# Kernel tuning notes

Measured on AMD Instinct MI355X. Metric: run time of the kernel, lower is better.

## Reference

```python
import jax, jax.numpy as jnp
import numpy as np

C = 64
B, H, W = 2, 128, 512
SCALE = C ** (-0.5)


def conv1x1(x, w, b):
    # x: [B,C,H,W], w: [O,I], b: [O]
    return jnp.einsum('bihw,oi->bohw', x, w) + b[None, :, None, None]


def dwconv3x3(x, w, b):
    # depthwise 3x3, w: [C,1,3,3]
    y = jax.lax.conv_general_dilated(
        x, w, window_strides=(1, 1), padding='SAME',
        feature_group_count=x.shape[1],
        dimension_numbers=('NCHW', 'OIHW', 'NCHW'))
    return y + b[None, :, None, None]


def proj12(x, w1, b1, wd, bd):
    return dwconv3x3(conv1x1(x, w1, b1), wd, bd)


def setup_inputs() -> dict:
    key = jax.random.key(0)
    ks = jax.random.split(key, 32)
    d = {}
    d['x_l'] = jax.random.normal(ks[0], (B, C, H, W), dtype=jnp.float32)
    d['x_r'] = jax.random.normal(ks[1], (B, C, H, W), dtype=jnp.float32)
    i = 2
    for p in ['lp1', 'rp1', 'lp2', 'rp2']:
        d[p + '_w1'] = jax.random.normal(ks[i], (C, C), dtype=jnp.float32) * 0.05; i += 1
        d[p + '_b1'] = jnp.zeros((C,), dtype=jnp.float32)
        d[p + '_wd'] = jax.random.normal(ks[i], (C, 1, 3, 3), dtype=jnp.float32) * 0.1; i += 1
        d[p + '_bd'] = jnp.zeros((C,), dtype=jnp.float32)
    for p in ['lp3', 'rp3']:
        d[p + '_w'] = jax.random.normal(ks[i], (C, C), dtype=jnp.float32) * 0.05; i += 1
        d[p + '_b'] = jnp.zeros((C,), dtype=jnp.float32)
    return d


def reference(x_l, x_r,
              lp1_w1, lp1_b1, lp1_wd, lp1_bd,
              rp1_w1, rp1_b1, rp1_wd, rp1_bd,
              lp2_w1, lp2_b1, lp2_wd, lp2_bd,
              rp2_w1, rp2_b1, rp2_wd, rp2_bd,
              lp3_w, lp3_b, rp3_w, rp3_b):
    Ql = proj12(x_l, lp1_w1, lp1_b1, lp1_wd, lp1_bd)  # [B,C,H,W]
    Qr = proj12(x_r, rp1_w1, rp1_b1, rp1_wd, rp1_bd)  # [B,C,H,W]
    # attention[b,h,w,v] = sum_c Ql[b,c,h,w] * Qr[b,c,h,v]
    att = jnp.einsum('bchw,bchv->bhwv', Ql, Qr) * SCALE  # [B,H,W,W]
    Vl = proj12(x_l, lp2_w1, lp2_b1, lp2_wd, lp2_bd)
    Vr = proj12(x_r, rp2_w1, rp2_b1, rp2_wd, rp2_bd)
    # softmax over right-view width (last axis), aggregate Vr
    A_r2l = jax.nn.softmax(att, axis=-1)
    F_r2l = jnp.einsum('bhwv,bchv->bchw', A_r2l, Vr)  # [B,C,H,W]
    # transposed attention, softmax over left-view width (axis -2 of att)
    A_l2r = jax.nn.softmax(att, axis=-2)
    F_l2r = jnp.einsum('bhwv,bchw->bchv', A_l2r, Vl)  # [B,C,H,W]
    F_r2l = conv1x1(F_r2l, lp3_w, lp3_b)
    F_l2r = conv1x1(F_l2r, rp3_w, rp3_b)
    return x_l + F_r2l + x_r + F_l2r
```

## Files before the change

### kernel.cpp

```cpp
#include <hip/hip_runtime.h>
#include <hip/hip_bf16.h>

typedef __attribute__((ext_vector_type(8))) short short8;
typedef __attribute__((ext_vector_type(4))) float f32x4;

#define QSCALE 0.18033688011112042f

__device__ __forceinline__ unsigned short f2bf(float f){
    unsigned u = __float_as_uint(f);
    unsigned r = (u + 0x7fffu + ((u>>16)&1u))>>16;
    return (unsigned short)r;
}
__device__ __forceinline__ unsigned pk_rtne(float hi, float lo){
    return (((unsigned)f2bf(hi))<<16) | (unsigned)f2bf(lo);
}

__global__ __launch_bounds__(256) void prepgemm_k(const float* __restrict__ xl,
                                                  const float* __restrict__ xr,
                                                  float* __restrict__ out,
                                                  const float* __restrict__ wAL, const float* __restrict__ bAL,
                                                  const float* __restrict__ wBL, const float* __restrict__ bBL,
                                                  const float* __restrict__ wAR, const float* __restrict__ bAR,
                                                  const float* __restrict__ wBR, const float* __restrict__ bBR,
                                                  unsigned short* __restrict__ T1L, unsigned short* __restrict__ T2L,
                                                  unsigned short* __restrict__ T1R, unsigned short* __restrict__ T2R){
    __shared__ float ftA[64*130];
    __shared__ __align__(16) short sB[128*72];
    __shared__ float sbias[128];

    int bid = blockIdx.x;
    int b = bid >> 9, px0 = (bid & 511) << 7;
    int tid = threadIdx.x;
    int wv = tid>>6, lane = tid&63, quad = lane>>4, l16 = lane&15;

    float4 vxr[8];
    #pragma unroll
    for (int it=0; it<8; it++){
        int lin = it*256 + tid;
        int c = lin >> 5, piece = lin & 31;
        size_t off = (((size_t)(b*64 + c))<<16) + px0 + piece*4;
        float4 va = *(const float4*)(xl + off);
        float4 vb = *(const float4*)(xr + off);
        vxr[it] = vb;
        float4 vo; vo.x=va.x+vb.x; vo.y=va.y+vb.y; vo.z=va.z+vb.z; vo.w=va.w+vb.w;
        *(float4*)(out + off) = vo;
        float* d = ftA + c*130 + piece*4;
        float2 lo; lo.x=va.x; lo.y=va.y;
        float2 hi; hi.x=va.z; hi.y=va.w;
        *(float2*)(d) = lo;
        *(float2*)(d+2) = hi;
    }
    {
        #pragma unroll
        for (int it=0; it<8; it++){
            int lin = it*256 + tid;
            int o = lin >> 4, cc4 = (lin & 15) << 2;
            const float* wsrc = (o < 64) ? (wAL + o*64 + cc4) : (wBL + (o-64)*64 + cc4);
            float4 w4 = *(const float4*)wsrc;
            uint2 v; v.x = pk_rtne(w4.y, w4.x); v.y = pk_rtne(w4.w, w4.z);
            *(uint2*)(sB + o*72 + cc4) = v;
        }
        if (tid < 128) sbias[tid] = (tid < 64) ? bAL[tid] : bBL[tid-64];
    }
    __syncthreads();

    const f32x4 z4 = {0.f,0.f,0.f,0.f};

    #define DO_GEMM(T1p, T2p) do {                                                  \
        short8 a0[2], a1[2];                                                        \
        _Pragma("unroll")                                                           \
        for (int mt=0; mt<2; mt++){                                                 \
            int pxr = wv*32 + mt*16 + l16;                                          \
            _Pragma("unroll")                                                       \
            for (int j=0;j<8;j++){                                                  \
                a0[mt][j] = (short)f2bf(ftA[(quad*8 + j)*130 + pxr]);               \
                a1[mt][j] = (short)f2bf(ftA[(32 + quad*8 + j)*130 + pxr]);          \
            }                                                                       \
        }                                                                           \
        _Pragma("unroll")                                                           \
        for (int set=0; set<2; set++){                                              \
            unsigned short* T = set ? (T2p) : (T1p);                                \
            short8 bB0[4], bB1[4];                                                  \
            _Pragma("unroll")                                                       \
            for (int nt=0; nt<4; nt++){                                             \
                bB0[nt] = *(const short8*)(sB + (set*64 + nt*16 + l16)*72 + quad*8);      \
                bB1[nt] = *(const short8*)(sB + (set*64 + nt*16 + l16)*72 + 32 + quad*8); \
            }                                                                       \
            _Pragma("unroll")                                                       \
            for (int nt=0; nt<4; nt++){                                             \
                float4 b4 = *(const float4*)(sbias + set*64 + nt*16 + quad*4);      \
                _Pragma("unroll")                                                   \
                for (int mt=0; mt<2; mt++){                                         \
                    f32x4 acc = __builtin_amdgcn_mfma_f32_16x16x32_bf16(bB0[nt], a0[mt], z4, 0,0,0); \
                    acc       = __builtin_amdgcn_mfma_f32_16x16x32_bf16(bB1[nt], a1[mt], acc, 0,0,0); \
                    uint2 v;                                                        \
                    v.x = pk_rtne(acc[1]+b4.y, acc[0]+b4.x);                        \
                    v.y = pk_rtne(acc[3]+b4.w, acc[2]+b4.z);                        \
                    int px = px0 + wv*32 + mt*16 + l16;                             \
                    *(uint2*)(T + (size_t)px*64 + nt*16 + quad*4) = v;              \
                }                                                                   \
            }                                                                       \
        }                                                                           \
    } while(0)

    DO_GEMM(T1L + ((size_t)b<<22), T2L + ((size_t)b<<22));
    __syncthreads();

    #pragma unroll
    for (int it=0; it<8; it++){
        int lin = it*256 + tid;
        int c = lin >> 5, piece = lin & 31;
        float4 vb = vxr[it];
        float* d = ftA + c*130 + piece*4;
        float2 lo; lo.x=vb.x; lo.y=vb.y;
        float2 hi; hi.x=vb.z; hi.y=vb.w;
        *(float2*)(d) = lo;
        *(float2*)(d+2) = hi;
    }
    {
        #pragma unroll
        for (int it=0; it<8; it++){
            int lin = it*256 + tid;
            int o = lin >> 4, cc4 = (lin & 15) << 2;
            const float* wsrc = (o < 64) ? (wAR + o*64 + cc4) : (wBR + (o-64)*64 + cc4);
            float4 w4 = *(const float4*)wsrc;
            uint2 v; v.x = pk_rtne(w4.y, w4.x); v.y = pk_rtne(w4.w, w4.z);
            *(uint2*)(sB + o*72 + cc4) = v;
        }
        if (tid < 128) sbias[tid] = (tid < 64) ? bAR[tid] : bBR[tid-64];
    }
    __syncthreads();

    DO_GEMM(T1R + ((size_t)b<<22), T2R + ((size_t)b<<22));
    #undef DO_GEMM
}

__device__ __forceinline__ void dw_tile(const unsigned short* __restrict__ Tb,
                                        const float* __restrict__ wd,
                                        const float* __restrict__ bd,
                                        int c0, int w0, int h, float acc[4][4]){
    #pragma unroll
    for (int ch=0; ch<4; ch++){
        float bv = bd[c0+ch];
        #pragma unroll
        for (int i=0;i<4;i++) acc[ch][i] = bv;
    }
    #pragma unroll
    for (int dh=-1; dh<=1; dh++){
        int hh = h + dh;
        if (hh < 0 || hh > 127) continue;
        const unsigned short* Tr = Tb + ((size_t)(hh*512))*64 + c0;
        float win[6][4];
        #pragma unroll
        for (int j=0;j<6;j++){
            int ww = w0 - 1 + j;
            if (ww >= 0 && ww < 512){
                uint2 v = *(const uint2*)(Tr + (size_t)ww*64);
                win[j][0] = __uint_as_float(v.x<<16);
                win[j][1] = __uint_as_float(v.x & 0xffff0000u);
                win[j][2] = __uint_as_float(v.y<<16);
                win[j][3] = __uint_as_float(v.y & 0xffff0000u);
            } else {
                win[j][0]=0.f; win[j][1]=0.f; win[j][2]=0.f; win[j][3]=0.f;
            }
        }
        #pragma unroll
        for (int ch=0; ch<4; ch++){
            float k0 = wd[(c0+ch)*9 + (dh+1)*3];
            float k1 = wd[(c0+ch)*9 + (dh+1)*3 + 1];
            float k2 = wd[(c0+ch)*9 + (dh+1)*3 + 2];
            #pragma unroll
            for (int i=0;i<4;i++)
                acc[ch][i] += k0*win[i][ch] + k1*win[i+1][ch] + k2*win[i+2][ch];
        }
    }
}

__global__ __launch_bounds__(256) void dwconv_k(const unsigned short* __restrict__ T1,
                                                const unsigned short* __restrict__ T2,
                                                const float* __restrict__ wd1,
                                                const float* __restrict__ bd1,
                                                const float* __restrict__ wd2,
                                                const float* __restrict__ bd2,
                                                unsigned short* __restrict__ Qdst,
                                                unsigned short* __restrict__ Vdst,
                                                float qscale){
    int bid = blockIdx.x;
    int wt = bid & 7, h = (bid>>3)&127, b = bid>>10;
    int tid = threadIdx.x;
    int cg = tid & 15, wl = tid >> 4;
    int c0 = cg*4;
    int w0 = wt*64 + wl*4;
    float acc[4][4];
    dw_tile(T1 + ((size_t)b<<22), wd1, bd1, c0, w0, h, acc);
    {
        int base = (b*128 + h)*512;
        #pragma unroll
        for (int i=0;i<4;i++){
            uint2 v;
            v.x = pk_rtne(acc[1][i]*qscale, acc[0][i]*qscale);
            v.y = pk_rtne(acc[3][i]*qscale, acc[2][i]*qscale);
            *(uint2*)(Qdst + ((size_t)(base + w0 + i))*64 + c0) = v;
        }
    }
    dw_tile(T2 + ((size_t)b<<22), wd2, bd2, c0, w0, h, acc);
    {
        #pragma unroll
        for (int ch=0; ch<4; ch++){
            uint2 v;
            v.x = pk_rtne(acc[ch][1], acc[ch][0]);
            v.y = pk_rtne(acc[ch][3], acc[ch][2]);
            *(uint2*)(Vdst + (((size_t)(b*64 + c0 + ch))<<16) + h*512 + w0) = v;
        }
    }
}

#define PQ 72
#define PK 72
#define PV 72
#define PP 72
#define PFA 72
#define POT 17
#define OFF_Q   0
#define OFF_K   18432
#define OFF_V   27648
#define LDS_TOT 36864

__global__ __launch_bounds__(256) void flash_k(
    const unsigned short* __restrict__ Ql, const unsigned short* __restrict__ Qr,
    const unsigned short* __restrict__ Vl, const unsigned short* __restrict__ Vr,
    const float* __restrict__ lw3, const float* __restrict__ lb3,
    const float* __restrict__ rw3, const float* __restrict__ rb3,
    float* __restrict__ out)
{
    __shared__ __align__(16) char smem[LDS_TOT];
    short* sK  = (short*)(smem + OFF_K);
    short* sV  = (short*)(smem + OFF_V);
    short* sP  = (short*)(smem + OFF_Q);
    short* sFA = (short*)(smem + OFF_Q);
    float* sOT = (float*)(smem + OFF_K);

    int bid = blockIdx.x;
    int g  = ((bid >> 5) << 3) | (bid & 7);
    int qt = (bid >> 3) & 3;
    int h = g & 127, b = (g >> 7) & 1, dir = g >> 8;
    const unsigned short *Qg, *Kg, *Vg; const float *w3, *b3;
    if (dir==0){ Qg = Ql; Kg = Qr; Vg = Vr; w3 = lw3; b3 = lb3; }
    else       { Qg = Qr; Kg = Ql; Vg = Vl; w3 = rw3; b3 = rb3; }

    int tid = threadIdx.x;
    int wv = tid>>6, lane = tid&63, quad = lane>>4, l16 = lane&15;
    int bh = b*128 + h;

    short8 aq0[2], aq1[2];
    #pragma unroll
    for (int s=0; s<2; s++){
        size_t qrow = ((size_t)bh*512 + qt*128 + wv*32 + s*16 + l16)*64;
        aq0[s] = *(const short8*)(Qg + qrow + quad*8);
        aq1[s] = *(const short8*)(Qg + qrow + 32 + quad*8);
    }

    const f32x4 z4 = {0.f,0.f,0.f,0.f};
    f32x4 oacc[2][4];
    #pragma unroll
    for (int s=0; s<2; s++)
        #pragma unroll
        for (int ct=0; ct<4; ct++) oacc[s][ct] = z4;
    float lps[2] = {0.f, 0.f};

    const uint4* Ksrc = (const uint4*)(Kg + (size_t)bh*512*64);
    const unsigned short* Vbase = Vg + ((size_t)(b*64)*128 + h)*512;

    for (int kt=0; kt<8; kt++){
        #pragma unroll
        for (int it=0; it<2; it++){
            int idx = it*256 + tid;
            int row = idx>>3, piece = idx&7;
            *(uint4*)(sK + row*PK + piece*8) = Ksrc[(size_t)(kt*64 + row)*8 + piece];
            uint4 vv = *(const uint4*)(Vbase + (size_t)row*65536 + kt*64 + piece*8);
            *(uint4*)(sV + row*PV + piece*8) = vv;
        }
        __syncthreads();
        #pragma unroll
        for (int nt=0; nt<4; nt++){
            short8 bk0 = *(const short8*)(sK + (nt*16 + l16)*PK + quad*8);
            short8 bk1 = *(const short8*)(sK + (nt*16 + l16)*PK + 32 + quad*8);
            #pragma unroll
            for (int s=0; s<2; s++){
                __builtin_amdgcn_s_setprio(1);
                f32x4 sv = __builtin_amdgcn_mfma_f32_16x16x32_bf16(bk0, aq0[s], z4, 0,0,0);
                sv       = __builtin_amdgcn_mfma_f32_16x16x32_bf16(bk1, aq1[s], sv, 0,0,0);
                __builtin_amdgcn_s_setprio(0);
                float p0 = __builtin_amdgcn_exp2f(sv[0]);
                float p1 = __builtin_amdgcn_exp2f(sv[1]);
                float p2 = __builtin_amdgcn_exp2f(sv[2]);
                float p3 = __builtin_amdgcn_exp2f(sv[3]);
                lps[s] += (p0+p1) + (p2+p3);
                unsigned lo = __builtin_amdgcn_perm(__float_as_uint(p1), __float_as_uint(p0), 0x07060302);
                unsigned hi = __builtin_amdgcn_perm(__float_as_uint(p3), __float_as_uint(p2), 0x07060302);
                uint2 pv; pv.x = lo; pv.y = hi;
                *(uint2*)(sP + (wv*32 + s*16 + l16)*PP + nt*16 + quad*4) = pv;
            }
        }
        short8 ap0[2], ap1[2];
        #pragma unroll
        for (int s=0; s<2; s++){
            ap0[s] = *(const short8*)(sP + (wv*32 + s*16 + l16)*PP + quad*8);
            ap1[s] = *(const short8*)(sP + (wv*32 + s*16 + l16)*PP + 32 + quad*8);
        }
        __builtin_amdgcn_s_setprio(1);
        #pragma unroll
        for (int ct=0; ct<4; ct++){
            short8 bv0 = *(const short8*)(sV + (ct*16 + l16)*PV + quad*8);
            short8 bv1 = *(const short8*)(sV + (ct*16 + l16)*PV + 32 + quad*8);
            #pragma unroll
            for (int s=0; s<2; s++){
                oacc[s][ct] = __builtin_amdgcn_mfma_f32_16x16x32_bf16(ap0[s], bv0, oacc[s][ct], 0,0,0);
                oacc[s][ct] = __builtin_amdgcn_mfma_f32_16x16x32_bf16(ap1[s], bv1, oacc[s][ct], 0,0,0);
            }
        }
        __builtin_amdgcn_s_setprio(0);
        __syncthreads();
    }

    float inv[2][4];
    #pragma unroll
    for (int s=0; s<2; s++){
        float l = lps[s];
        l += __shfl_xor(l, 16);
        l += __shfl_xor(l, 32);
        #pragma unroll
        for (int r=0;r<4;r++) inv[s][r] = 1.0f / __shfl(l, quad*4 + r);
    }

    #pragma unroll
    for (int s=0; s<2; s++){
        short* sFw = sFA + (wv*32 + s*16)*PFA;
        #pragma unroll
        for (int ct=0; ct<4; ct++){
            #pragma unroll
            for (int r=0;r<4;r++)
                sFw[(quad*4+r)*PFA + ct*16 + l16] = (short)f2bf(oacc[s][ct][r]*inv[s][r]);
        }
    }
    short8 af0[2], af1[2];
    #pragma unroll
    for (int s=0; s<2; s++){
        af0[s] = *(const short8*)(sFA + (wv*32 + s*16 + l16)*PFA + quad*8);
        af1[s] = *(const short8*)(sFA + (wv*32 + s*16 + l16)*PFA + 32 + quad*8);
    }
    f32x4 d2[2][4];
    #pragma unroll
    for (int ot=0; ot<4; ot++){
        const float* wrow = w3 + (ot*16 + l16)*64 + quad*8;
        float4 wa = *(const float4*)(wrow);
        float4 wb = *(const float4*)(wrow + 4);
        float4 wc = *(const float4*)(wrow + 32);
        float4 wd = *(const float4*)(wrow + 36);
        short8 bw0, bw1;
        bw0[0]=(short)f2bf(wa.x); bw0[1]=(short)f2bf(wa.y); bw0[2]=(short)f2bf(wa.z); bw0[3]=(short)f2bf(wa.w);
        bw0[4]=(short)f2bf(wb.x); bw0[5]=(short)f2bf(wb.y); bw0[6]=(short)f2bf(wb.z); bw0[7]=(short)f2bf(wb.w);
        bw1[0]=(short)f2bf(wc.x); bw1[1]=(short)f2bf(wc.y); bw1[2]=(short)f2bf(wc.z); bw1[3]=(short)f2bf(wc.w);
        bw1[4]=(short)f2bf(wd.x); bw1[5]=(short)f2bf(wd.y); bw1[6]=(short)f2bf(wd.z); bw1[7]=(short)f2bf(wd.w);
        float bias = b3[ot*16 + l16];
        #pragma unroll
        for (int s=0; s<2; s++){
            d2[s][ot] = __builtin_amdgcn_mfma_f32_16x16x32_bf16(af0[s], bw0, z4, 0,0,0);
            d2[s][ot] = __builtin_amdgcn_mfma_f32_16x16x32_bf16(af1[s], bw1, d2[s][ot], 0,0,0);
            #pragma unroll
            for (int r=0;r<4;r++) d2[s][ot][r] += bias;
        }
    }
    float* sOw = sOT + wv*(64*POT);
    #pragma unroll
    for (int s=0; s<2; s++){
        #pragma unroll
        for (int ot=0; ot<4; ot++){
            #pragma unroll
            for (int r=0;r<4;r++)
                sOw[(ot*16 + l16)*POT + quad*4 + r] = d2[s][ot][r];
        }
        int qbase = qt*128 + wv*32 + s*16;
        #pragma unroll
        for (int it=0; it<16; it++){
            int o = it*4 + quad;
            float val = sOw[o*POT + l16];
            unsafeAtomicAdd(out + ((size_t)(b*64 + o)*128 + h)*512 + qbase + l16, val);
        }
    }
}

extern "C" void kernel_launch(void* const* d_in, const int* in_sizes, int n_in,
                              void* d_out, int out_size, void* d_ws, size_t ws_size,
                              hipStream_t stream)
{
    const float* xl = (const float*)d_in[0];
    const float* xr = (const float*)d_in[1];
    const float* lp1_w1 = (const float*)d_in[2];
    const float* lp1_b1 = (const float*)d_in[3];
    const float* lp1_wd = (const float*)d_in[4];
    const float* lp1_bd = (const float*)d_in[5];
    const float* rp1_w1 = (const float*)d_in[6];
    const float* rp1_b1 = (const float*)d_in[7];
    const float* rp1_wd = (const float*)d_in[8];
    const float* rp1_bd = (const float*)d_in[9];
    const float* lp2_w1 = (const float*)d_in[10];
    const float* lp2_b1 = (const float*)d_in[11];
    const float* lp2_wd = (const float*)d_in[12];
    const float* lp2_bd = (const float*)d_in[13];
    const float* rp2_w1 = (const float*)d_in[14];
    const float* rp2_b1 = (const float*)d_in[15];
    const float* rp2_wd = (const float*)d_in[16];
    const float* rp2_bd = (const float*)d_in[17];
    const float* lp3_w  = (const float*)d_in[18];
    const float* lp3_b  = (const float*)d_in[19];
    const float* rp3_w  = (const float*)d_in[20];
    const float* rp3_b  = (const float*)d_in[21];
    float* out = (float*)d_out;

    const size_t S = 16777216;
    char* ws = (char*)d_ws;
    unsigned short* s0 = (unsigned short*)(ws);
    unsigned short* s1 = (unsigned short*)(ws + 1*S);
    unsigned short* s2 = (unsigned short*)(ws + 2*S);
    unsigned short* s3 = (unsigned short*)(ws + 3*S);
    unsigned short* s4 = (unsigned short*)(ws + 4*S);
    unsigned short* s5 = (unsigned short*)(ws + 5*S);

    prepgemm_k<<<1024, 256, 0, stream>>>(xl, xr, out,
        lp1_w1, lp1_b1, lp2_w1, lp2_b1,
        rp1_w1, rp1_b1, rp2_w1, rp2_b1,
        s2, s3, s4, s5);

    dwconv_k<<<2048, 256, 0, stream>>>(s2, s3,
        lp1_wd, lp1_bd, lp2_wd, lp2_bd, s0, s1, QSCALE);

    dwconv_k<<<2048, 256, 0, stream>>>(s4, s5,
        rp1_wd, rp1_bd, rp2_wd, rp2_bd, s2, s3, 1.0f);

    flash_k<<<2048, 256, 0, stream>>>(s0, s2, s1, s3,
        lp3_w, lp3_b, rp3_w, rp3_b, out);
}
```

Before: 309.0 us.

## Load K and V fragments directly from global memory, dropping LDS staging

The flash kernel no longer stages each 64-row K and V tile through shared memory. Each wave now loads its own MFMA B-operand fragments straight from global memory into registers, and both per-iteration __syncthreads barriers are removed. This cuts LDS traffic, LDS footprint and block-wide synchronisation. The cost is that all four waves fetch the same K/V data, which quadruples cache-level load traffic, and global-load latency is now exposed right before the MFMAs with no explicit prefetch.

```diff
diff --git a/kernel.cpp b/kernel.cpp
--- a/kernel.cpp
+++ b/kernel.cpp
@@ -215,16 +215,12 @@
     }
 }
 
-#define PQ 72
-#define PK 72
-#define PV 72
 #define PP 72
 #define PFA 72
 #define POT 17
-#define OFF_Q   0
-#define OFF_K   18432
-#define OFF_V   27648
-#define LDS_TOT 36864
+#define OFF_P   0
+#define OFF_OT  18432
+#define LDS_TOT 35840
 
 __global__ __launch_bounds__(256) void flash_k(
     const unsigned short* __restrict__ Ql, const unsigned short* __restrict__ Qr,
@@ -234,11 +230,9 @@
     float* __restrict__ out)
 {
     __shared__ __align__(16) char smem[LDS_TOT];
-    short* sK  = (short*)(smem + OFF_K);
-    short* sV  = (short*)(smem + OFF_V);
-    short* sP  = (short*)(smem + OFF_Q);
-    short* sFA = (short*)(smem + OFF_Q);
-    float* sOT = (float*)(smem + OFF_K);
+    short* sP  = (short*)(smem + OFF_P);
+    short* sFA = (short*)(smem + OFF_P);
+    float* sOT = (float*)(smem + OFF_OT);
 
     int bid = blockIdx.x;
     int g  = ((bid >> 5) << 3) | (bid & 7);
@@ -268,28 +262,24 @@
         for (int ct=0; ct<4; ct++) oacc[s][ct] = z4;
     float lps[2] = {0.f, 0.f};
 
-    const uint4* Ksrc = (const uint4*)(Kg + (size_t)bh*512*64);
+    const unsigned short* Kbase = Kg + (size_t)bh*512*64;
     const unsigned short* Vbase = Vg + ((size_t)(b*64)*128 + h)*512;
 
     for (int kt=0; kt<8; kt++){
-        #pragma unroll
-        for (int it=0; it<2; it++){
-            int idx = it*256 + tid;
-            int row = idx>>3, piece = idx&7;
-            *(uint4*)(sK + row*PK + piece*8) = Ksrc[(size_t)(kt*64 + row)*8 + piece];
-            uint4 vv = *(const uint4*)(Vbase + (size_t)row*65536 + kt*64 + piece*8);
-            *(uint4*)(sV + row*PV + piece*8) = vv;
-        }
-        __syncthreads();
+        short8 bk0[4], bk1[4];
         #pragma unroll
         for (int nt=0; nt<4; nt++){
-            short8 bk0 = *(const short8*)(sK + (nt*16 + l16)*PK + quad*8);
-            short8 bk1 = *(const short8*)(sK + (nt*16 + l16)*PK + 32 + quad*8);
+            const unsigned short* kr = Kbase + (size_t)(kt*64 + nt*16 + l16)*64;
+            bk0[nt] = *(const short8*)(kr + quad*8);
+            bk1[nt] = *(const short8*)(kr + 32 + quad*8);
+        }
+        #pragma unroll
+        for (int nt=0; nt<4; nt++){
             #pragma unroll
             for (int s=0; s<2; s++){
                 __builtin_amdgcn_s_setprio(1);
-                f32x4 sv = __builtin_amdgcn_mfma_f32_16x16x32_bf16(bk0, aq0[s], z4, 0,0,0);
-                sv       = __builtin_amdgcn_mfma_f32_16x16x32_bf16(bk1, aq1[s], sv, 0,0,0);
+                f32x4 sv = __builtin_amdgcn_mfma_f32_16x16x32_bf16(bk0[nt], aq0[s], z4, 0,0,0);
+                sv       = __builtin_amdgcn_mfma_f32_16x16x32_bf16(bk1[nt], aq1[s], sv, 0,0,0);
                 __builtin_amdgcn_s_setprio(0);
                 float p0 = __builtin_amdgcn_exp2f(sv[0]);
                 float p1 = __builtin_amdgcn_exp2f(sv[1]);
@@ -311,8 +301,9 @@
         __builtin_amdgcn_s_setprio(1);
         #pragma unroll
         for (int ct=0; ct<4; ct++){
-            short8 bv0 = *(const short8*)(sV + (ct*16 + l16)*PV + quad*8);
-            short8 bv1 = *(const short8*)(sV + (ct*16 + l16)*PV + 32 + quad*8);
+            const unsigned short* vr = Vbase + (size_t)(ct*16 + l16)*65536 + kt*64;
+            short8 bv0 = *(const short8*)(vr + quad*8);
+            short8 bv1 = *(const short8*)(vr + 32 + quad*8);
             #pragma unroll
             for (int s=0; s<2; s++){
                 oacc[s][ct] = __builtin_amdgcn_mfma_f32_16x16x32_bf16(ap0[s], bv0, oacc[s][ct], 0,0,0);
@@ -320,7 +311,6 @@
             }
         }
         __builtin_amdgcn_s_setprio(0);
-        __syncthreads();
     }
 
     float inv[2][4];
```

Result: slower. 392.9 us (+27.2%).

## Process four output rows per dwconv block with a rolling row window

Applied to the files above, without the earlier changes.

Each dwconv block now computes HB=4 consecutive output rows. It keeps a three-row register ring buffer so each input row is loaded once and reused across the vertical taps, instead of being reloaded three times. Weights and biases are hoisted into registers once per block, and the grid shrinks from 2048 to 512 blocks. The trade is higher register pressure and fewer blocks, which could lower occupancy or leave the GPU underfilled on a dwconv that is a small part of the whole pipeline.

```diff
diff --git a/kernel.cpp b/kernel.cpp
--- a/kernel.cpp
+++ b/kernel.cpp
@@ -135,47 +135,46 @@
     #undef DO_GEMM
 }
 
-__device__ __forceinline__ void dw_tile(const unsigned short* __restrict__ Tb,
-                                        const float* __restrict__ wd,
-                                        const float* __restrict__ bd,
-                                        int c0, int w0, int h, float acc[4][4]){
+__device__ __forceinline__ void dw_loadrow(const unsigned short* __restrict__ Tb,
+                                           int c0, int w0, int hh, float win[6][4]){
+    if (hh < 0 || hh > 127){
+        #pragma unroll
+        for (int j=0;j<6;j++){ win[j][0]=0.f; win[j][1]=0.f; win[j][2]=0.f; win[j][3]=0.f; }
+        return;
+    }
+    const unsigned short* Tr = Tb + ((size_t)(hh*512))*64 + c0;
+    #pragma unroll
+    for (int j=0;j<6;j++){
+        int ww = w0 - 1 + j;
+        if (ww >= 0 && ww < 512){
+            uint2 v = *(const uint2*)(Tr + (size_t)ww*64);
+            win[j][0] = __uint_as_float(v.x<<16);
+            win[j][1] = __uint_as_float(v.x & 0xffff0000u);
+            win[j][2] = __uint_as_float(v.y<<16);
+            win[j][3] = __uint_as_float(v.y & 0xffff0000u);
+        } else {
+            win[j][0]=0.f; win[j][1]=0.f; win[j][2]=0.f; win[j][3]=0.f;
+        }
+    }
+}
+
+__device__ __forceinline__ void dw_conv3(const float kw[4][9], const float bv4[4],
+                                         const float rA[6][4], const float rB[6][4],
+                                         const float rC[6][4], float acc[4][4]){
     #pragma unroll
     for (int ch=0; ch<4; ch++){
-        float bv = bd[c0+ch];
-        #pragma unroll
-        for (int i=0;i<4;i++) acc[ch][i] = bv;
-    }
-    #pragma unroll
-    for (int dh=-1; dh<=1; dh++){
-        int hh = h + dh;
-        if (hh < 0 || hh > 127) continue;
-        const unsigned short* Tr = Tb + ((size_t)(hh*512))*64 + c0;
-        float win[6][4];
-        #pragma unroll
-        for (int j=0;j<6;j++){
-            int ww = w0 - 1 + j;
-            if (ww >= 0 && ww < 512){
-                uint2 v = *(const uint2*)(Tr + (size_t)ww*64);
-                win[j][0] = __uint_as_float(v.x<<16);
-                win[j][1] = __uint_as_float(v.x & 0xffff0000u);
-                win[j][2] = __uint_as_float(v.y<<16);
-                win[j][3] = __uint_as_float(v.y & 0xffff0000u);
-            } else {
-                win[j][0]=0.f; win[j][1]=0.f; win[j][2]=0.f; win[j][3]=0.f;
-            }
-        }
-        #pragma unroll
-        for (int ch=0; ch<4; ch++){
-            float k0 = wd[(c0+ch)*9 + (dh+1)*3];
-            float k1 = wd[(c0+ch)*9 + (dh+1)*3 + 1];
-            float k2 = wd[(c0+ch)*9 + (dh+1)*3 + 2];
-            #pragma unroll
-            for (int i=0;i<4;i++)
-                acc[ch][i] += k0*win[i][ch] + k1*win[i+1][ch] + k2*win[i+2][ch];
-        }
-    }
-}
-
+        #pragma unroll
+        for (int i=0;i<4;i++){
+            float a = bv4[ch];
+            a += kw[ch][0]*rA[i][ch] + kw[ch][1]*rA[i+1][ch] + kw[ch][2]*rA[i+2][ch];
+            a += kw[ch][3]*rB[i][ch] + kw[ch][4]*rB[i+1][ch] + kw[ch][5]*rB[i+2][ch];
+            a += kw[ch][6]*rC[i][ch] + kw[ch][7]*rC[i+1][ch] + kw[ch][8]*rC[i+2][ch];
+            acc[ch][i] = a;
+        }
+    }
+}
+
+#define HB 4
 __global__ __launch_bounds__(256) void dwconv_k(const unsigned short* __restrict__ T1,
                                                 const unsigned short* __restrict__ T2,
                                                 const float* __restrict__ wd1,
@@ -186,31 +185,73 @@
                                                 unsigned short* __restrict__ Vdst,
                                                 float qscale){
     int bid = blockIdx.x;
-    int wt = bid & 7, h = (bid>>3)&127, b = bid>>10;
+    int wt = bid & 7, hb = (bid>>3)&31, b = bid>>8;
     int tid = threadIdx.x;
     int cg = tid & 15, wl = tid >> 4;
     int c0 = cg*4;
     int w0 = wt*64 + wl*4;
-    float acc[4][4];
-    dw_tile(T1 + ((size_t)b<<22), wd1, bd1, c0, w0, h, acc);
+    int h0 = hb*HB;
+
     {
-        int base = (b*128 + h)*512;
-        #pragma unroll
-        for (int i=0;i<4;i++){
-            uint2 v;
-            v.x = pk_rtne(acc[1][i]*qscale, acc[0][i]*qscale);
-            v.y = pk_rtne(acc[3][i]*qscale, acc[2][i]*qscale);
-            *(uint2*)(Qdst + ((size_t)(base + w0 + i))*64 + c0) = v;
-        }
-    }
-    dw_tile(T2 + ((size_t)b<<22), wd2, bd2, c0, w0, h, acc);
+        const unsigned short* Tb = T1 + ((size_t)b<<22);
+        float kw[4][9], bv4[4];
+        #pragma unroll
+        for (int ch=0; ch<4; ch++){
+            bv4[ch] = bd1[c0+ch];
+            #pragma unroll
+            for (int t=0;t<9;t++) kw[ch][t] = wd1[(c0+ch)*9 + t];
+        }
+        float rw0[6][4], rw1[6][4], rw2[6][4];
+        dw_loadrow(Tb, c0, w0, h0-1, rw0);
+        dw_loadrow(Tb, c0, w0, h0  , rw1);
+        float acc[4][4];
+        #pragma unroll
+        for (int hh=0; hh<HB; hh++){
+            float (*rA)[4] = (hh%3==0)? rw0 : (hh%3==1)? rw1 : rw2;
+            float (*rB)[4] = (hh%3==0)? rw1 : (hh%3==1)? rw2 : rw0;
+            float (*rC)[4] = (hh%3==0)? rw2 : (hh%3==1)? rw0 : rw1;
+            dw_loadrow(Tb, c0, w0, h0+hh+1, rC);
+            dw_conv3(kw, bv4, rA, rB, rC, acc);
+            int h = h0 + hh;
+            int base = (b*128 + h)*512;
+            #pragma unroll
+            for (int i=0;i<4;i++){
+                uint2 v;
+                v.x = pk_rtne(acc[1][i]*qscale, acc[0][i]*qscale);
+                v.y = pk_rtne(acc[3][i]*qscale, acc[2][i]*qscale);
+                *(uint2*)(Qdst + ((size_t)(base + w0 + i))*64 + c0) = v;
+            }
+        }
+    }
+
     {
+        const unsigned short* Tb = T2 + ((size_t)b<<22);
+        float kw[4][9], bv4[4];
         #pragma unroll
         for (int ch=0; ch<4; ch++){
-            uint2 v;
-            v.x = pk_rtne(acc[ch][1], acc[ch][0]);
-            v.y = pk_rtne(acc[ch][3], acc[ch][2]);
-            *(uint2*)(Vdst + (((size_t)(b*64 + c0 + ch))<<16) + h*512 + w0) = v;
+            bv4[ch] = bd2[c0+ch];
+            #pragma unroll
+            for (int t=0;t<9;t++) kw[ch][t] = wd2[(c0+ch)*9 + t];
+        }
+        float rw0[6][4], rw1[6][4], rw2[6][4];
+        dw_loadrow(Tb, c0, w0, h0-1, rw0);
+        dw_loadrow(Tb, c0, w0, h0  , rw1);
+        float acc[4][4];
+        #pragma unroll
+        for (int hh=0; hh<HB; hh++){
+            float (*rA)[4] = (hh%3==0)? rw0 : (hh%3==1)? rw1 : rw2;
+            float (*rB)[4] = (hh%3==0)? rw1 : (hh%3==1)? rw2 : rw0;
+            float (*rC)[4] = (hh%3==0)? rw2 : (hh%3==1)? rw0 : rw1;
+            dw_loadrow(Tb, c0, w0, h0+hh+1, rC);
+            dw_conv3(kw, bv4, rA, rB, rC, acc);
+            int h = h0 + hh;
+            #pragma unroll
+            for (int ch=0; ch<4; ch++){
+                uint2 v;
+                v.x = pk_rtne(acc[ch][1], acc[ch][0]);
+                v.y = pk_rtne(acc[ch][3], acc[ch][2]);
+                *(uint2*)(Vdst + (((size_t)(b*64 + c0 + ch))<<16) + h*512 + w0) = v;
+            }
         }
     }
 }
@@ -432,10 +473,10 @@
         rp1_w1, rp1_b1, rp2_w1, rp2_b1,
         s2, s3, s4, s5);
 
-    dwconv_k<<<2048, 256, 0, stream>>>(s2, s3,
+    dwconv_k<<<512, 256, 0, stream>>>(s2, s3,
         lp1_wd, lp1_bd, lp2_wd, lp2_bd, s0, s1, QSCALE);
 
-    dwconv_k<<<2048, 256, 0, stream>>>(s4, s5,
+    dwconv_k<<<512, 256, 0, stream>>>(s4, s5,
         rp1_wd, rp1_bd, rp2_wd, rp2_bd, s2, s3, 1.0f);
 
     flash_k<<<2048, 256, 0, stream>>>(s0, s2, s1, s3,
```

Result: no change. 303.3 us (-1.8%).
